# Optimization experiments

Hardware: AMD Instinct MI355X
Metric: run time of the kernel (lower is better)

The kernel has to match this reference:

```python
import jax, jax.numpy as jnp
import numpy as np

SEQ, B, V, D = 512, 128, 32000, 1024


def setup_inputs() -> dict:
    key = jax.random.key(0)
    ks = jax.random.split(key, 10)
    s = 1.0 / np.sqrt(D).astype(np.float32)  # torch LSTMCell init scale
    x = jax.random.randint(ks[0], (SEQ, B), 0, V)
    emb = jax.random.normal(ks[1], (V, D), jnp.float32).at[0].set(0.0)  # padding_idx=0
    W_ih = jax.random.uniform(ks[2], (4 * D, D), jnp.float32, -s, s)
    W_hh = jax.random.uniform(ks[3], (4 * D, D), jnp.float32, -s, s)
    b_ih = jax.random.uniform(ks[4], (4 * D,), jnp.float32, -s, s)
    b_hh = jax.random.uniform(ks[5], (4 * D,), jnp.float32, -s, s)
    h0 = jax.random.normal(ks[6], (D,), jnp.float32)
    c0 = jax.random.normal(ks[7], (D,), jnp.float32)
    h0_2 = jax.random.normal(ks[8], (D,), jnp.float32)
    c0_2 = jax.random.normal(ks[9], (D,), jnp.float32)
    return {"x": x, "emb": emb, "W_ih": W_ih, "W_hh": W_hh, "b_ih": b_ih,
            "b_hh": b_hh, "h0": h0, "c0": c0, "h0_2": h0_2, "c0_2": c0_2}


def _lstm_cell(xt, h, c, W_ih, W_hh, b_ih, b_hh):
    # torch.nn.LSTMCell gate order: i, f, g, o
    gates = xt @ W_ih.T + b_ih + h @ W_hh.T + b_hh  # [B, 4D]
    i, f, g, o = jnp.split(gates, 4, axis=-1)
    c_new = jax.nn.sigmoid(f) * c + jax.nn.sigmoid(i) * jnp.tanh(g)
    h_new = jax.nn.sigmoid(o) * jnp.tanh(c_new)
    return h_new, c_new


def reference(x, emb, W_ih, W_hh, b_ih, b_hh, h0, c0, h0_2, c0_2):
    batch = x.shape[1]
    e = emb[x]  # [S, B, D] (time-major, like the torch loop over embed)
    h = jnp.broadcast_to(h0, (batch, h0.shape[0]))
    c = jnp.broadcast_to(c0, (batch, c0.shape[0]))
    h2 = jnp.broadcast_to(h0_2, (batch, h0_2.shape[0]))
    c2 = jnp.broadcast_to(c0_2, (batch, c0_2.shape[0]))

    def step(carry, inp):
        h, c, h2, c2 = carry
        et, raw = inp
        pad = (raw == 0)[:, None]  # [B, 1]
        h1, c1 = _lstm_cell(et, h, c, W_ih, W_hh, b_ih, b_hh)
        h2n, c2n = _lstm_cell(h1, h2, c2, W_ih, W_hh, b_ih, b_hh)
        # faithful to source: layer-2 state also falls back to layer-1 pre-state on pads
        h_new = jnp.where(pad, h, h1)
        c_new = jnp.where(pad, c, c1)
        h2_new = jnp.where(pad, h, h2n)
        c2_new = jnp.where(pad, c, c2n)
        return (h_new, c_new, h2_new, c2_new), None

    (h, c, h2, c2), _ = jax.lax.scan(step, (h, c, h2, c2), (e, x))
    return (h, c, h2, c2)
```

## Files before the change

### kernel.cpp

```cpp
#include <hip/hip_runtime.h>
#include <hip/hip_bf16.h>
#include <stdint.h>

#define SEQ   512
#define BATCH 128
#define DIM   1024
#define BD    (BATCH * DIM)
#define NBLK  256
#define LDS_BYTES 131072

typedef __bf16 bf16x8 __attribute__((ext_vector_type(8)));
typedef float  f32x4  __attribute__((ext_vector_type(4)));

__device__ __forceinline__ float sigf(float x) { return 1.0f / (1.0f + __expf(-x)); }

__device__ __forceinline__ bf16x8 pack_f32(float4 a, float4 b) {
    bf16x8 r;
    r[0] = (__bf16)a.x; r[1] = (__bf16)a.y; r[2] = (__bf16)a.z; r[3] = (__bf16)a.w;
    r[4] = (__bf16)b.x; r[5] = (__bf16)b.y; r[6] = (__bf16)b.z; r[7] = (__bf16)b.w;
    return r;
}
__device__ __forceinline__ bf16x8 ld_b16x8(const __hip_bfloat16* p) {
    uint4 u = *reinterpret_cast<const uint4*>(p);
    return __builtin_bit_cast(bf16x8, u);
}
__device__ __forceinline__ void st_dev_bf16(__hip_bfloat16* p, float v) {
    unsigned short u = __builtin_bit_cast(unsigned short, (__bf16)v);
    __hip_atomic_store((unsigned short*)p, u, __ATOMIC_RELAXED, __HIP_MEMORY_SCOPE_AGENT);
}
__device__ __forceinline__ void st_row8(__hip_bfloat16* p, float v, int jj) {
    float v1 = __shfl_down(v, 1);
    float v2 = __shfl_down(v, 2);
    float v3 = __shfl_down(v, 3);
    if ((jj & 3) == 0) {
        union { unsigned short s[4]; unsigned long long u; } q;
        q.s[0] = __builtin_bit_cast(unsigned short, (__bf16)v);
        q.s[1] = __builtin_bit_cast(unsigned short, (__bf16)v1);
        q.s[2] = __builtin_bit_cast(unsigned short, (__bf16)v2);
        q.s[3] = __builtin_bit_cast(unsigned short, (__bf16)v3);
        __hip_atomic_store((unsigned long long*)p, q.u, __ATOMIC_RELAXED,
                           __HIP_MEMORY_SCOPE_AGENT);
    }
}
__device__ __forceinline__ unsigned ld_sc(const unsigned* p) {
    return __hip_atomic_load(p, __ATOMIC_RELAXED, __HIP_MEMORY_SCOPE_AGENT);
}
__device__ __forceinline__ void st_sc(unsigned* p, unsigned v) {
    __hip_atomic_store(p, v, __ATOMIC_RELAXED, __HIP_MEMORY_SCOPE_AGENT);
}
__device__ __forceinline__ unsigned rmw_sc(unsigned* p) {
    return __hip_atomic_fetch_add(p, 1u, __ATOMIC_RELAXED, __HIP_MEMORY_SCOPE_AGENT);
}

__device__ __forceinline__ void gsync(unsigned* scd, int cg) {
    __syncthreads();
    if (threadIdx.x == 0) {
        const int g = cg & 7;
        unsigned* genl = scd + (24 + g) * 16;
        unsigned gen = ld_sc(genl);
        const unsigned p = gen & 1u;
        unsigned* ga = scd + (p * 8 + g) * 16;
        if (rmw_sc(ga) == 7u) {
            st_sc(ga, 0u);
            unsigned* tp = scd + (16 + p) * 16;
            if (rmw_sc(tp) == 7u) {
                st_sc(tp, 0u);
#pragma unroll
                for (int i = 0; i < 8; ++i)
                    st_sc(scd + (24 + i) * 16, gen + 1u);
            } else {
                while (ld_sc(genl) == gen) __builtin_amdgcn_s_sleep(1);
            }
        } else {
            while (ld_sc(genl) == gen) __builtin_amdgcn_s_sleep(1);
        }
        __builtin_amdgcn_fence(__ATOMIC_ACQUIRE, "agent");
    }
    __syncthreads();
}

__device__ __forceinline__ void load_h_frags(bf16x8 (&afr)[2][8],
    const __hip_bfloat16* Ab, size_t aoff0, size_t aoff1)
{
#pragma unroll
    for (int kc = 0; kc < 8; ++kc) {
        afr[0][kc] = ld_b16x8(Ab + aoff0 + kc * 32);
        afr[1][kc] = ld_b16x8(Ab + aoff1 + kc * 32);
    }
}
__device__ __forceinline__ void load_emb_frags(bf16x8 (&afr)[2][8],
    const float* e0, const float* e1)
{
#pragma unroll
    for (int kc = 0; kc < 8; ++kc) {
        afr[0][kc] = pack_f32(*(const float4*)(e0 + kc * 32),
                              *(const float4*)(e0 + kc * 32 + 4));
        afr[1][kc] = pack_f32(*(const float4*)(e1 + kc * 32),
                              *(const float4*)(e1 + kc * 32 + 4));
    }
}

__device__ __forceinline__ void mfma_all(const bf16x8 (&afr)[2][8],
    const bf16x8 (&breg)[4][8], f32x4 (&acc)[2][4])
{
#pragma unroll
    for (int kc = 0; kc < 8; ++kc)
#pragma unroll
        for (int mt = 0; mt < 2; ++mt)
#pragma unroll
            for (int nt = 0; nt < 4; ++nt)
                acc[mt][nt] = __builtin_amdgcn_mfma_f32_16x16x32_bf16(
                    afr[mt][kc], breg[nt][kc], acc[mt][nt], 0, 0, 0);
}

__device__ __forceinline__ void write_part(float* part, const f32x4 (&acc)[2][4],
    int w, int quad, int l16)
{
#pragma unroll
    for (int mt = 0; mt < 2; ++mt)
#pragma unroll
        for (int nt = 0; nt < 4; ++nt) {
            int n  = nt * 16 + l16;
            int a  = ((n >> 2) & 7) ^ ((n & 3) << 1);
            int dw = w * 2048 + n * 32 + ((mt * 16 + quad * 4) ^ (a << 2));
            *(f32x4*)(part + dw) = acc[mt][nt];
        }
}
__device__ __forceinline__ void read_part(const float* part, int rr, int jj, float (&g4)[4])
{
    g4[0] = g4[1] = g4[2] = g4[3] = 0.f;
#pragma unroll
    for (int wv = 0; wv < 8; ++wv)
#pragma unroll
        for (int g = 0; g < 4; ++g) {
            int a = ((jj & 7) ^ (g << 1));
            g4[g] += part[wv * 2048 + (jj * 4 + g) * 32 + (rr ^ (a << 2))];
        }
}

__global__ __launch_bounds__(512, 2) void lstm_persist(
    const int* __restrict__ x, const float* __restrict__ emb,
    const float* __restrict__ Wih, const float* __restrict__ Whh,
    const float* __restrict__ bih, const float* __restrict__ bhh,
    const float* __restrict__ h0, const float* __restrict__ c0,
    const float* __restrict__ h02, const float* __restrict__ c02,
    __hip_bfloat16* __restrict__ hbase, unsigned* __restrict__ sync,
    float* __restrict__ out)
{
    extern __shared__ float lds[];
    float* partA = lds;
    float* partB = lds + 16384;

    const int tid  = threadIdx.x;
    const int w    = tid >> 6;
    const int lane = tid & 63;
    const int quad = lane >> 4;
    const int l16  = lane & 15;
    const int s    = w & 1;
    const int kq   = w >> 1;
    const int cg   = blockIdx.x & 63;
    const int mqh  = blockIdx.x >> 6;
    const int R0   = mqh * 32;
    const int J0   = cg * 16;
    const int rr   = tid >> 4;
    const int jj   = tid & 15;
    const int col  = J0 + jj;
    const int grow = R0 + rr;
    const size_t off = (size_t)grow * DIM + col;

    const int arow0 = R0 + l16;
    const int arow1 = R0 + 16 + l16;
    const int kb    = kq * 256 + quad * 8;
    const size_t aoff0 = (size_t)arow0 * DIM + kb;
    const size_t aoff1 = (size_t)arow1 * DIM + kb;

    unsigned* scd = sync + (mqh << 10);

    __hip_bfloat16* hbf0  = hbase;
    __hip_bfloat16* hbf1  = hbase + BD;
    __hip_bfloat16* h1bf0 = hbase + 2 * BD;
    __hip_bfloat16* h1bf1 = hbase + 3 * BD;
    __hip_bfloat16* h2bf0 = hbase + 4 * BD;
    __hip_bfloat16* h2bf1 = hbase + 5 * BD;

    bf16x8 breg[4][8];
    {
        const float* Wm = s ? Whh : Wih;
#pragma unroll
        for (int nt = 0; nt < 4; ++nt) {
            int n = nt * 16 + l16;
            const float* wp = Wm + (size_t)((n & 3) * DIM + J0 + (n >> 2)) * DIM + kb;
#pragma unroll
            for (int kc = 0; kc < 8; ++kc)
                breg[nt][kc] = pack_f32(*(const float4*)(wp + kc * 32),
                                        *(const float4*)(wp + kc * 32 + 4));
        }
    }

    float hc  = h0[col],  cc1 = c0[col];
    float hp  = hc,       cp  = cc1;
    float h2f = h02[col], c2f = c02[col];
    float bias[4];
#pragma unroll
    for (int g = 0; g < 4; ++g) bias[g] = bih[g * DIM + col] + bhh[g * DIM + col];

    int ta0 = x[arow0], ta1 = x[arow1];
    int gxc = x[grow];
    int gxp = 0;

    st_dev_bf16(hbf1 + off, hc);
    st_dev_bf16(h2bf1 + off, h2f);
    gsync(scd, cg);

#pragma unroll 1
    for (int t = 0; t <= SEQ; ++t) {
        bf16x8 afr1[2][8];
        if (t >= 1) {
            const __hip_bfloat16* Ab = (s == 0)
                ? (((t - 1) & 1) ? h1bf1 : h1bf0)
                : ((t & 1) ? h2bf1 : h2bf0);
            bf16x8 afr2[2][8];
            load_h_frags(afr2, Ab, aoff0, aoff1);
            f32x4 acc[2][4];
#pragma unroll
            for (int mt = 0; mt < 2; ++mt)
#pragma unroll
                for (int nt = 0; nt < 4; ++nt) acc[mt][nt] = (f32x4)(0.f);
            mfma_all(afr2, breg, acc);
            if (t < SEQ) {
                if (s == 0)
                    load_emb_frags(afr1, emb + (size_t)ta0 * DIM + kb,
                                         emb + (size_t)ta1 * DIM + kb);
                else
                    load_h_frags(afr1, ((t + 1) & 1) ? hbf1 : hbf0, aoff0, aoff1);
            }
            write_part(partA, acc, w, quad, l16);
        } else {
            if (s == 0)
                load_emb_frags(afr1, emb + (size_t)ta0 * DIM + kb,
                                     emb + (size_t)ta1 * DIM + kb);
            else
                load_h_frags(afr1, hbf1, aoff0, aoff1);
        }
        __syncthreads();
        if (t >= 1) {
            float g4[4]; read_part(partA, rr, jj, g4);
            float gi = g4[0] + bias[0], gf = g4[1] + bias[1];
            float gg = g4[2] + bias[2], go = g4[3] + bias[3];
            float cn = sigf(gf) * c2f + sigf(gi) * tanhf(gg);
            float hn = sigf(go) * tanhf(cn);
            bool pad = (gxp == 0);
            h2f = pad ? hp : hn;
            c2f = pad ? cp : cn;
            st_row8((((t - 1) & 1) ? h2bf1 : h2bf0) + (off & ~(size_t)3), h2f, jj);
        }
        if (t < SEQ) {
            f32x4 acc[2][4];
#pragma unroll
            for (int mt = 0; mt < 2; ++mt)
#pragma unroll
                for (int nt = 0; nt < 4; ++nt) acc[mt][nt] = (f32x4)(0.f);
            mfma_all(afr1, breg, acc);
            write_part(partB, acc, w, quad, l16);
            __syncthreads();
            float g4[4]; read_part(partB, rr, jj, g4);
            float gi = g4[0] + bias[0], gf = g4[1] + bias[1];
            float gg = g4[2] + bias[2], go = g4[3] + bias[3];
            float cn = sigf(gf) * cc1 + sigf(gi) * tanhf(gg);
            float hn = sigf(go) * tanhf(cn);
            bool pad = (gxc == 0);
            float hm = pad ? hc : hn;
            float cm = pad ? cc1 : cn;
            st_row8(((t & 1) ? h1bf1 : h1bf0) + (off & ~(size_t)3), hn, jj);
            st_row8(((t & 1) ? hbf1 : hbf0) + (off & ~(size_t)3), hm, jj);
            hp = hc; cp = cc1; hc = hm; cc1 = cm;
            gxp = gxc;
            int tn = (t + 1 < SEQ) ? t + 1 : t;
            gxc = x[tn * BATCH + grow];
            ta0 = x[tn * BATCH + arow0];
            ta1 = x[tn * BATCH + arow1];
            gsync(scd, cg);
        }
    }

    out[0 * BD + off] = hc;
    out[1 * BD + off] = cc1;
    out[2 * BD + off] = h2f;
    out[3 * BD + off] = c2f;
}

__global__ void zero_sync_k(unsigned* sc) {
    sc[blockIdx.x * blockDim.x + threadIdx.x] = 0u;
}

extern "C" void kernel_launch(void* const* d_in, const int* in_sizes, int n_in,
                              void* d_out, int out_size, void* d_ws, size_t ws_size,
                              hipStream_t stream) {
    (void)in_sizes; (void)n_in; (void)out_size; (void)ws_size;
    const int*   x    = (const int*)d_in[0];
    const float* emb  = (const float*)d_in[1];
    const float* Wih  = (const float*)d_in[2];
    const float* Whh  = (const float*)d_in[3];
    const float* bih  = (const float*)d_in[4];
    const float* bhh  = (const float*)d_in[5];
    const float* h0   = (const float*)d_in[6];
    const float* c0   = (const float*)d_in[7];
    const float* h02  = (const float*)d_in[8];
    const float* c02  = (const float*)d_in[9];

    unsigned* sync = (unsigned*)d_ws;
    __hip_bfloat16* hbase = (__hip_bfloat16*)((char*)d_ws + 16384);
    float* outp = (float*)d_out;

    static int attr_done = 0;
    if (!attr_done) {
        (void)hipFuncSetAttribute((const void*)lstm_persist,
                                  hipFuncAttributeMaxDynamicSharedMemorySize, LDS_BYTES);
        attr_done = 1;
    }

    zero_sync_k<<<8, 512, 0, stream>>>(sync);

    void* args[] = { (void*)&x, (void*)&emb, (void*)&Wih, (void*)&Whh,
                     (void*)&bih, (void*)&bhh, (void*)&h0, (void*)&c0,
                     (void*)&h02, (void*)&c02, (void*)&hbase, (void*)&sync,
                     (void*)&outp };
    hipError_t e = hipLaunchCooperativeKernel((const void*)lstm_persist,
                                              dim3(NBLK), dim3(512), args,
                                              (unsigned)LDS_BYTES, stream);
    if (e != hipSuccess) {
        lstm_persist<<<NBLK, 512, LDS_BYTES, stream>>>(
            x, emb, Wih, Whh, bih, bhh, h0, c0, h02, c02, hbase, sync, outp);
    }
}
```

Measured before the change: 11.90 ms.

## Replace hierarchical grid barrier with per-block flags and stage embeddings in LDS

Swaps the atomic-counter tree barrier for monotonic per-block step flags that each block publishes and a single wavefront polls with a vote. After publishing its flag, each block gathers the next step's embedding rows into a swizzled bf16 LDS buffer, so the fetch runs off the critical path. tanhf is replaced by an exp-based fast tanh. The LDS buffer reuses the partB region, and the flag scheme assumes a monotonic counter and layout, which brings a risk of ordering bugs.

```diff
diff --git a/kernel.cpp b/kernel.cpp
--- a/kernel.cpp
+++ b/kernel.cpp
@@ -13,6 +13,10 @@
 typedef float  f32x4  __attribute__((ext_vector_type(4)));
 
 __device__ __forceinline__ float sigf(float x) { return 1.0f / (1.0f + __expf(-x)); }
+__device__ __forceinline__ float fast_tanh(float x) {
+    float e = __expf(2.0f * x);
+    return 1.0f - 2.0f / (e + 1.0f);
+}
 
 __device__ __forceinline__ bf16x8 pack_f32(float4 a, float4 b) {
     bf16x8 r;
@@ -48,34 +52,17 @@
 __device__ __forceinline__ void st_sc(unsigned* p, unsigned v) {
     __hip_atomic_store(p, v, __ATOMIC_RELAXED, __HIP_MEMORY_SCOPE_AGENT);
 }
-__device__ __forceinline__ unsigned rmw_sc(unsigned* p) {
-    return __hip_atomic_fetch_add(p, 1u, __ATOMIC_RELAXED, __HIP_MEMORY_SCOPE_AGENT);
-}
-
-__device__ __forceinline__ void gsync(unsigned* scd, int cg) {
-    __syncthreads();
-    if (threadIdx.x == 0) {
-        const int g = cg & 7;
-        unsigned* genl = scd + (24 + g) * 16;
-        unsigned gen = ld_sc(genl);
-        const unsigned p = gen & 1u;
-        unsigned* ga = scd + (p * 8 + g) * 16;
-        if (rmw_sc(ga) == 7u) {
-            st_sc(ga, 0u);
-            unsigned* tp = scd + (16 + p) * 16;
-            if (rmw_sc(tp) == 7u) {
-                st_sc(tp, 0u);
-#pragma unroll
-                for (int i = 0; i < 8; ++i)
-                    st_sc(scd + (24 + i) * 16, gen + 1u);
-            } else {
-                while (ld_sc(genl) == gen) __builtin_amdgcn_s_sleep(1);
-            }
-        } else {
-            while (ld_sc(genl) == gen) __builtin_amdgcn_s_sleep(1);
-        }
+
+__device__ __forceinline__ void flag_wait(unsigned* scd, unsigned thr) {
+    if (threadIdx.x < 64) {
+        for (;;) {
+            unsigned v = ld_sc(scd + threadIdx.x * 4);
+            if (__all((int)(v >= thr))) break;
+            __builtin_amdgcn_s_sleep(2);
+        }
+    }
+    if (threadIdx.x == 0)
         __builtin_amdgcn_fence(__ATOMIC_ACQUIRE, "agent");
-    }
     __syncthreads();
 }
 
@@ -88,15 +75,31 @@
         afr[1][kc] = ld_b16x8(Ab + aoff1 + kc * 32);
     }
 }
-__device__ __forceinline__ void load_emb_frags(bf16x8 (&afr)[2][8],
-    const float* e0, const float* e1)
-{
-#pragma unroll
-    for (int kc = 0; kc < 8; ++kc) {
-        afr[0][kc] = pack_f32(*(const float4*)(e0 + kc * 32),
-                              *(const float4*)(e0 + kc * 32 + 4));
-        afr[1][kc] = pack_f32(*(const float4*)(e1 + kc * 32),
-                              *(const float4*)(e1 + kc * 32 + 4));
+
+__device__ __forceinline__ void ebuf_read_frags(bf16x8 (&afr)[2][8],
+    const char* ebuf, int kq, int quad, int l16)
+{
+#pragma unroll
+    for (int mt = 0; mt < 2; ++mt) {
+        int r = mt * 16 + l16;
+        const char* base = ebuf + r * 2048;
+        int sw = r & 7;
+#pragma unroll
+        for (int kc = 0; kc < 8; ++kc) {
+            int cb = kq * 32 + kc * 4 + quad;
+            afr[mt][kc] = *(const bf16x8*)(base + ((cb ^ sw) * 16));
+        }
+    }
+}
+__device__ __forceinline__ void ebuf_fill(char* ebuf, int er, int ecb, const float* ep)
+{
+    char* base = ebuf + er * 2048;
+    int sw = er & 7;
+#pragma unroll
+    for (int i = 0; i < 8; ++i) {
+        float4 a = *(const float4*)(ep + i * 8);
+        float4 b = *(const float4*)(ep + i * 8 + 4);
+        *(bf16x8*)(base + (((ecb + i) ^ sw) * 16)) = pack_f32(a, b);
     }
 }
 
@@ -150,6 +153,7 @@
     extern __shared__ float lds[];
     float* partA = lds;
     float* partB = lds + 16384;
+    char*  ebuf  = (char*)(lds + 16384);
 
     const int tid  = threadIdx.x;
     const int w    = tid >> 6;
@@ -167,6 +171,8 @@
     const int col  = J0 + jj;
     const int grow = R0 + rr;
     const size_t off = (size_t)grow * DIM + col;
+    const int er   = tid >> 4;
+    const int ecb  = (tid & 15) * 8;
 
     const int arow0 = R0 + l16;
     const int arow1 = R0 + 16 + l16;
@@ -204,55 +210,54 @@
 #pragma unroll
     for (int g = 0; g < 4; ++g) bias[g] = bih[g * DIM + col] + bhh[g * DIM + col];
 
-    int ta0 = x[arow0], ta1 = x[arow1];
     int gxc = x[grow];
     int gxp = 0;
 
     st_dev_bf16(hbf1 + off, hc);
     st_dev_bf16(h2bf1 + off, h2f);
-    gsync(scd, cg);
+    {
+        int tok = x[R0 + er];
+        ebuf_fill(ebuf, er, ecb, emb + (size_t)tok * DIM + ecb * 8);
+    }
+    __syncthreads();
+    if (tid == 0) st_sc(scd + cg * 4, 1u);
 
 #pragma unroll 1
     for (int t = 0; t <= SEQ; ++t) {
-        bf16x8 afr1[2][8];
+        flag_wait(scd, (unsigned)(t + 1));
+        bf16x8 afr[2][8];
         if (t >= 1) {
             const __hip_bfloat16* Ab = (s == 0)
                 ? (((t - 1) & 1) ? h1bf1 : h1bf0)
                 : ((t & 1) ? h2bf1 : h2bf0);
-            bf16x8 afr2[2][8];
-            load_h_frags(afr2, Ab, aoff0, aoff1);
+            load_h_frags(afr, Ab, aoff0, aoff1);
             f32x4 acc[2][4];
 #pragma unroll
             for (int mt = 0; mt < 2; ++mt)
 #pragma unroll
                 for (int nt = 0; nt < 4; ++nt) acc[mt][nt] = (f32x4)(0.f);
-            mfma_all(afr2, breg, acc);
+            mfma_all(afr, breg, acc);
             if (t < SEQ) {
-                if (s == 0)
-                    load_emb_frags(afr1, emb + (size_t)ta0 * DIM + kb,
-                                         emb + (size_t)ta1 * DIM + kb);
-                else
-                    load_h_frags(afr1, ((t + 1) & 1) ? hbf1 : hbf0, aoff0, aoff1);
+                if (s == 1) load_h_frags(afr, ((t + 1) & 1) ? hbf1 : hbf0, aoff0, aoff1);
+                else        ebuf_read_frags(afr, ebuf, kq, quad, l16);
             }
             write_part(partA, acc, w, quad, l16);
+            __syncthreads();
+            {
+                float g4[4]; read_part(partA, rr, jj, g4);
+                float gi = g4[0] + bias[0], gf = g4[1] + bias[1];
+                float gg = g4[2] + bias[2], go = g4[3] + bias[3];
+                float cn = sigf(gf) * c2f + sigf(gi) * fast_tanh(gg);
+                float hn = sigf(go) * fast_tanh(cn);
+                bool pad = (gxp == 0);
+                h2f = pad ? hp : hn;
+                c2f = pad ? cp : cn;
+                st_row8((((t - 1) & 1) ? h2bf1 : h2bf0) + (off & ~(size_t)3), h2f, jj);
+            }
         } else {
-            if (s == 0)
-                load_emb_frags(afr1, emb + (size_t)ta0 * DIM + kb,
-                                     emb + (size_t)ta1 * DIM + kb);
-            else
-                load_h_frags(afr1, hbf1, aoff0, aoff1);
-        }
-        __syncthreads();
-        if (t >= 1) {
-            float g4[4]; read_part(partA, rr, jj, g4);
-            float gi = g4[0] + bias[0], gf = g4[1] + bias[1];
-            float gg = g4[2] + bias[2], go = g4[3] + bias[3];
-            float cn = sigf(gf) * c2f + sigf(gi) * tanhf(gg);
-            float hn = sigf(go) * tanhf(cn);
-            bool pad = (gxp == 0);
-            h2f = pad ? hp : hn;
-            c2f = pad ? cp : cn;
-            st_row8((((t - 1) & 1) ? h2bf1 : h2bf0) + (off & ~(size_t)3), h2f, jj);
+            if (s == 1) load_h_frags(afr, hbf1, aoff0, aoff1);
+            else        ebuf_read_frags(afr, ebuf, kq, quad, l16);
+            __syncthreads();
         }
         if (t < SEQ) {
             f32x4 acc[2][4];
@@ -260,26 +265,31 @@
             for (int mt = 0; mt < 2; ++mt)
 #pragma unroll
                 for (int nt = 0; nt < 4; ++nt) acc[mt][nt] = (f32x4)(0.f);
-            mfma_all(afr1, breg, acc);
+            mfma_all(afr, breg, acc);
             write_part(partB, acc, w, quad, l16);
             __syncthreads();
-            float g4[4]; read_part(partB, rr, jj, g4);
-            float gi = g4[0] + bias[0], gf = g4[1] + bias[1];
-            float gg = g4[2] + bias[2], go = g4[3] + bias[3];
-            float cn = sigf(gf) * cc1 + sigf(gi) * tanhf(gg);
-            float hn = sigf(go) * tanhf(cn);
-            bool pad = (gxc == 0);
-            float hm = pad ? hc : hn;
-            float cm = pad ? cc1 : cn;
-            st_row8(((t & 1) ? h1bf1 : h1bf0) + (off & ~(size_t)3), hn, jj);
-            st_row8(((t & 1) ? hbf1 : hbf0) + (off & ~(size_t)3), hm, jj);
-            hp = hc; cp = cc1; hc = hm; cc1 = cm;
-            gxp = gxc;
-            int tn = (t + 1 < SEQ) ? t + 1 : t;
-            gxc = x[tn * BATCH + grow];
-            ta0 = x[tn * BATCH + arow0];
-            ta1 = x[tn * BATCH + arow1];
-            gsync(scd, cg);
+            {
+                float g4[4]; read_part(partB, rr, jj, g4);
+                float gi = g4[0] + bias[0], gf = g4[1] + bias[1];
+                float gg = g4[2] + bias[2], go = g4[3] + bias[3];
+                float cn = sigf(gf) * cc1 + sigf(gi) * fast_tanh(gg);
+                float hn = sigf(go) * fast_tanh(cn);
+                bool pad = (gxc == 0);
+                float hm = pad ? hc : hn;
+                float cm = pad ? cc1 : cn;
+                st_row8(((t & 1) ? h1bf1 : h1bf0) + (off & ~(size_t)3), hn, jj);
+                st_row8(((t & 1) ? hbf1 : hbf0) + (off & ~(size_t)3), hm, jj);
+                hp = hc; cp = cc1; hc = hm; cc1 = cm;
+                gxp = gxc;
+            }
+            __syncthreads();
+            if (tid == 0) st_sc(scd + cg * 4, (unsigned)(t + 2));
+            if (t + 1 < SEQ) {
+                int tn = t + 1;
+                gxc = x[tn * BATCH + grow];
+                int tok = x[tn * BATCH + R0 + er];
+                ebuf_fill(ebuf, er, ecb, emb + (size_t)tok * DIM + ecb * 8);
+            }
         }
     }
 
```

New measurement: 9.808 ms. 1.21x faster.
